# Performance work log

Measured on AMD Instinct MI355X. Metric: run time of the kernel, lower is better.

The kernel has to match this reference:

```python
import jax, jax.numpy as jnp
import numpy as np

DIM = 768
HEADS = 8
HEAD_DIM = DIM // HEADS  # 96, divisible by 6 for 3-axis RoPE
ROPE_BASE = 10000.0


def rotary_pe_3d(x, coords):
    """Apply 3D-coordinate rotary embedding.
    x: [B, h, L, d] with d % 6 == 0; coords: [B, L, 3].
    Head dim is split into 3 equal blocks, one per spatial axis; each block
    gets rotate-half RoPE with angle = coord_axis * inv_freq.
    """
    B, h, L, d = x.shape
    d3 = d // 3
    half = d3 // 2
    inv_freq = 1.0 / (ROPE_BASE ** (jnp.arange(half, dtype=x.dtype) / half))  # [half]
    ang = coords[..., None] * inv_freq  # [B, L, 3, half]
    cos = jnp.cos(ang)[:, None]  # [B, 1, L, 3, half]
    sin = jnp.sin(ang)[:, None]
    xr = x.reshape(B, h, L, 3, d3)
    x1, x2 = xr[..., :half], xr[..., half:]
    out = jnp.concatenate([x1 * cos - x2 * sin, x1 * sin + x2 * cos], axis=-1)
    return out.reshape(B, h, L, d)


def setup_inputs() -> dict:
    key = jax.random.key(0)
    ks = jax.random.split(key, 9)
    B, Lq, Lk = 2, 2048, 2048
    s = DIM ** -0.5
    return {
        "Q_in": jax.random.normal(ks[0], (B, Lq, DIM), jnp.float32),
        "K_in": jax.random.normal(ks[1], (B, Lk, DIM), jnp.float32),
        "V_in": jax.random.normal(ks[2], (B, Lk, DIM), jnp.float32),
        "coords_q": jax.random.uniform(ks[3], (B, Lq, 3), jnp.float32) * 10.0,
        "coords_k": jax.random.uniform(ks[4], (B, Lk, 3), jnp.float32) * 10.0,
        "Wq": jax.random.normal(ks[5], (DIM, DIM), jnp.float32) * s,
        "Wk": jax.random.normal(ks[6], (DIM, DIM), jnp.float32) * s,
        "Wv": jax.random.normal(ks[7], (DIM, DIM), jnp.float32) * s,
        "Wo": jax.random.normal(ks[8], (DIM, DIM), jnp.float32) * s,
    }


def _split_heads(x, h):
    B, L, C = x.shape
    return x.reshape(B, L, h, C // h).transpose(0, 2, 1, 3)  # [B,h,L,d]


def reference(Q_in, K_in, V_in, coords_q, coords_k, Wq, Wk, Wv, Wo):
    scale = HEAD_DIM ** -0.5
    q = _split_heads(Q_in @ Wq.T, HEADS)
    k = _split_heads(K_in @ Wk.T, HEADS)
    v = _split_heads(V_in @ Wv.T, HEADS)
    q = rotary_pe_3d(q, coords_q)
    k = rotary_pe_3d(k, coords_k)
    attn = jnp.einsum('bhqd,bhkd->bhqk', q, k) * scale
    attn = jax.nn.softmax(attn, axis=-1)
    out = jnp.einsum('bhqk,bhkd->bhqd', attn, v)
    B, h, L, d = out.shape
    out = out.transpose(0, 2, 1, 3).reshape(B, L, h * d)
    return out @ Wo.T
```

## Files before the change

### kernel.cpp

```cpp
#include <hip/hip_runtime.h>
#include <stdint.h>

#define H 8
#define DH 96
#define L 2048
#define NB 2
#define D 768
#define ACTE 3145728
#define WELE 589824

typedef unsigned short u16;
typedef unsigned int u32;
typedef __attribute__((ext_vector_type(4))) __bf16 bf16x4;
typedef __attribute__((ext_vector_type(8))) __bf16 bf16x8;
typedef __attribute__((ext_vector_type(4))) float f32x4;
typedef __attribute__((ext_vector_type(16))) float f32x16;
typedef __attribute__((ext_vector_type(4))) u32 u32x4;
typedef __attribute__((ext_vector_type(2))) u32 u32x2;
typedef __attribute__((ext_vector_type(4))) u16 u16x4;

#define QSCALE 0.14724444f

static __device__ __forceinline__ u16 f2bf(float f) {
  union { __bf16 h; u16 u; } v;
  v.h = (__bf16)f;
  return v.u;
}

static __device__ __forceinline__ bf16x8 cvt8r(f32x4 a, f32x4 b) {
  bf16x8 r;
  r[0] = (__bf16)a[0]; r[1] = (__bf16)a[1]; r[2] = (__bf16)a[2]; r[3] = (__bf16)a[3];
  r[4] = (__bf16)b[0]; r[5] = (__bf16)b[1]; r[6] = (__bf16)b[2]; r[7] = (__bf16)b[3];
  return r;
}

static __device__ __forceinline__ void bar_lds() {
  asm volatile("s_waitcnt lgkmcnt(0)" ::: "memory");
  __builtin_amdgcn_s_barrier();
}

__global__ __launch_bounds__(256)
void cvt_bf16(const float* __restrict__ q, const float* __restrict__ k,
              const float* __restrict__ v, const float* __restrict__ wq,
              const float* __restrict__ wk, const float* __restrict__ wv,
              u16* __restrict__ dst)
{
  const long NCH = (3L * ACTE + 3L * WELE) / 8;
  for (long c = (long)blockIdx.x * 256 + threadIdx.x; c < NCH;
       c += (long)gridDim.x * 256) {
    long e = c * 8;
    const float* s;
    if (e < 3L * ACTE) {
      int t = (int)(e / ACTE);
      s = (t == 0 ? q : (t == 1 ? k : v)) + (e - (long)t * ACTE);
    } else {
      long e2 = e - 3L * ACTE;
      int t = (int)(e2 / WELE);
      s = (t == 0 ? wq : (t == 1 ? wk : wv)) + (e2 - (long)t * WELE);
    }
    f32x4 a = *(const f32x4*)s;
    f32x4 b = *(const f32x4*)(s + 4);
    *(bf16x8*)(dst + e) = cvt8r(a, b);
  }
}

__global__ __launch_bounds__(256, 3)
void proj_qkv_b(const u16* __restrict__ bfb,
                const float* __restrict__ cq, const float* __restrict__ ck,
                u16* __restrict__ qo, u16* __restrict__ ko, u16* __restrict__ vo)
{
  __shared__ __attribute__((aligned(16))) u16 a_lds[128 * 32];
  __shared__ __attribute__((aligned(16))) u16 b_lds[128 * 32];
  const int tid = threadIdx.x;
  const int lane = tid & 63;
  const int w = tid >> 6;
  const int wr = w >> 1, wc = w & 1;
  const int fr = lane & 15;
  const int hi = lane >> 4;

  const int f = blockIdx.x;
  const int xr = f & 7;
  const int g = f >> 3;
  const int z = g / 24;
  const int gg = g % 24;
  const int by = xr + 8 * (gg & 3);
  const int bx = gg >> 2;
  const int row0 = by * 128;
  const int col0 = bx * 128;

  const u16* A = bfb + (size_t)z * ACTE;
  const u16* W = bfb + 3L * ACTE + (size_t)z * WELE;

  f32x4 acc[4][4] = {};

  const int lrow = lane >> 2;
  const int lcol = (lane & 3) * 8;
  auto dma = [&](int k0) {
#pragma unroll
    for (int j = 0; j < 2; j++) {
      const int r0 = w * 32 + j * 16;
      const u16* gpa = A + (size_t)(row0 + r0 + lrow) * D + k0 + lcol;
      const u16* gpb = W + (size_t)(col0 + r0 + lrow) * D + k0 + lcol;
      __builtin_amdgcn_global_load_lds(
          (const __attribute__((address_space(1))) u32*)gpa,
          (__attribute__((address_space(3))) u32*)&a_lds[r0 * 32], 16, 0, 0);
      __builtin_amdgcn_global_load_lds(
          (const __attribute__((address_space(1))) u32*)gpb,
          (__attribute__((address_space(3))) u32*)&b_lds[r0 * 32], 16, 0, 0);
    }
  };

#pragma unroll 1
  for (int k0 = 0; k0 < D; k0 += 32) {
    dma(k0);
    __syncthreads();
    bf16x8 af[4], bf[4];
#pragma unroll
    for (int m = 0; m < 4; m++)
      af[m] = *(const bf16x8*)(&a_lds[(wr * 64 + m * 16 + fr) * 32 + hi * 8]);
#pragma unroll
    for (int n = 0; n < 4; n++)
      bf[n] = *(const bf16x8*)(&b_lds[(wc * 64 + n * 16 + fr) * 32 + hi * 8]);
#pragma unroll
    for (int m = 0; m < 4; m++)
#pragma unroll
      for (int n = 0; n < 4; n++)
        acc[m][n] = __builtin_amdgcn_mfma_f32_16x16x32_bf16(af[m], bf[n], acc[m][n], 0, 0, 0);
    __syncthreads();
  }

  if (z == 2) {
#pragma unroll
    for (int m = 0; m < 4; m++) {
      int rbase = row0 + wr * 64 + m * 16 + hi * 4;
#pragma unroll
      for (int n = 0; n < 4; n++) {
        int c = col0 + wc * 64 + n * 16 + fr;
        int hh = c / DH, dd = c % DH;
#pragma unroll
        for (int r = 0; r < 4; r++) {
          int row = rbase + r;
          int b = row >> 11, l = row & (L - 1);
          vo[((size_t)((b * H + hh) * DH + dd)) * L + l] = f2bf(acc[m][n][r]);
        }
      }
    }
  } else {
    const float* coords = (z == 0) ? cq : ck;
    u16* outp = (z == 0) ? qo : ko;
    const float postscale = (z == 0) ? QSCALE : 1.0f;
#pragma unroll
    for (int m = 0; m < 4; m++) {
      int rbase = row0 + wr * 64 + m * 16 + hi * 4;
#pragma unroll
      for (int np = 0; np < 2; np++) {
        int n1 = np * 2;
        int c1 = col0 + wc * 64 + n1 * 16 + fr;
        int hh = c1 / DH;
        int dd1 = c1 % DH;
        int axis = dd1 / 32;
        int j = dd1 & 15;
        float invf = exp2f(-(float)j * 0.83048202372184058f);
#pragma unroll
        for (int r = 0; r < 4; r++) {
          int row = rbase + r;
          int b = row >> 11, l = row & (L - 1);
          float coord = coords[((size_t)(b * L + l)) * 3 + axis];
          float ang = coord * invf;
          float sn = __sinf(ang), cs = __cosf(ang);
          float x1 = acc[m][n1][r], x2 = acc[m][n1 + 1][r];
          size_t base = ((size_t)((b * H + hh) * L + l)) * DH;
          outp[base + dd1] = f2bf((x1 * cs - x2 * sn) * postscale);
          outp[base + dd1 + 16] = f2bf((x1 * sn + x2 * cs) * postscale);
        }
      }
    }
  }
}

__global__ __launch_bounds__(256, 3)
void proj_qkv(const float* __restrict__ Qin, const float* __restrict__ Kin,
              const float* __restrict__ Vin,
              const float* __restrict__ Wq, const float* __restrict__ Wk,
              const float* __restrict__ Wv,
              const float* __restrict__ cq, const float* __restrict__ ck,
              u16* __restrict__ qo, u16* __restrict__ ko, u16* __restrict__ vo)
{
  __shared__ u16 a_lds[2][64 * 40];
  __shared__ u16 b_lds[2][192 * 40];
  const int tid = threadIdx.x;
  const int lane = tid & 63;
  const int w = tid >> 6;
  const int wr = w >> 1, wc = w & 1;
  const int fr = lane & 15;
  const int hi = lane >> 4;

  const int f = blockIdx.x;
  const int xcd = f & 7;
  const int g = f >> 3;
  const int bx = g & 3;
  const int h2 = g >> 2;
  const int byp = h2 & 7;
  const int z = h2 >> 3;
  const int by = xcd + 8 * byp;
  const int row0 = by * 64;
  const int col0 = bx * 192;

  const float* A = (z == 0) ? Qin : ((z == 1) ? Kin : Vin);
  const float* W = (z == 0) ? Wq : ((z == 1) ? Wk : Wv);

  const int arow = tid >> 2;
  const int acol = (tid & 3) * 8;
  const float* pA = A + (size_t)(row0 + arow) * D + acol;
  const float* pB0 = W + (size_t)(col0 + arow) * D + acol;
  const float* pB1 = pB0 + (size_t)64 * D;
  const float* pB2 = pB0 + (size_t)128 * D;

  f32x4 acc[2][6] = {};
  f32x4 Sa[2], Sb[6], Ta[2], Tb[6];

  auto issueP = [&](int k, f32x4* ra, f32x4* rb) {
    ra[0] = *(const f32x4*)(pA + k);
    ra[1] = *(const f32x4*)(pA + k + 4);
    rb[0] = *(const f32x4*)(pB0 + k);
    rb[1] = *(const f32x4*)(pB0 + k + 4);
    rb[2] = *(const f32x4*)(pB1 + k);
    rb[3] = *(const f32x4*)(pB1 + k + 4);
    rb[4] = *(const f32x4*)(pB2 + k);
    rb[5] = *(const f32x4*)(pB2 + k + 4);
  };
  auto stageP = [&](int bi, const f32x4* ra, const f32x4* rb) {
    *(bf16x8*)(&a_lds[bi][arow * 40 + acol]) = cvt8r(ra[0], ra[1]);
    *(bf16x8*)(&b_lds[bi][arow * 40 + acol]) = cvt8r(rb[0], rb[1]);
    *(bf16x8*)(&b_lds[bi][(arow + 64) * 40 + acol]) = cvt8r(rb[2], rb[3]);
    *(bf16x8*)(&b_lds[bi][(arow + 128) * 40 + acol]) = cvt8r(rb[4], rb[5]);
  };
  auto compute = [&](int bi) {
    bf16x8 af[2], bf[6];
#pragma unroll
    for (int m = 0; m < 2; m++)
      af[m] = *(const bf16x8*)(&a_lds[bi][(wr * 32 + m * 16 + fr) * 40 + hi * 8]);
#pragma unroll
    for (int n = 0; n < 6; n++)
      bf[n] = *(const bf16x8*)(&b_lds[bi][(wc * 96 + n * 16 + fr) * 40 + hi * 8]);
#pragma unroll
    for (int m = 0; m < 2; m++)
#pragma unroll
      for (int n = 0; n < 6; n++)
        acc[m][n] = __builtin_amdgcn_mfma_f32_16x16x32_bf16(af[m], bf[n], acc[m][n], 0, 0, 0);
  };

  issueP(0, Sa, Sb);
  stageP(0, Sa, Sb);
  issueP(32, Ta, Tb);
  bar_lds();

#pragma unroll 1
  for (int tt = 0; tt < 12; tt++) {
    const int k2 = tt * 64;
    if (k2 + 64 < D) issueP(k2 + 64, Sa, Sb);
    compute(0);
    stageP(1, Ta, Tb);
    bar_lds();
    if (k2 + 96 < D) issueP(k2 + 96, Ta, Tb);
    compute(1);
    if (k2 + 64 < D) stageP(0, Sa, Sb);
    bar_lds();
  }

  const int hh = (col0 + wc * 96) / DH;
  if (z == 2) {
#pragma unroll
    for (int m = 0; m < 2; m++) {
      int rbase = row0 + wr * 32 + m * 16 + hi * 4;
#pragma unroll
      for (int n = 0; n < 6; n++) {
        int dd = n * 16 + fr;
#pragma unroll
        for (int r = 0; r < 4; r++) {
          int row = rbase + r;
          int b = row >> 11, l = row & (L - 1);
          vo[((size_t)((b * H + hh) * DH + dd)) * L + l] = f2bf(acc[m][n][r]);
        }
      }
    }
  } else {
    const float* coords = (z == 0) ? cq : ck;
    u16* outp = (z == 0) ? qo : ko;
    const float postscale = (z == 0) ? QSCALE : 1.0f;
    const float invf = exp2f(-(float)fr * 0.83048202372184058f);
#pragma unroll
    for (int m = 0; m < 2; m++) {
      int rbase = row0 + wr * 32 + m * 16 + hi * 4;
#pragma unroll
      for (int np = 0; np < 3; np++) {
        int n1 = np * 2;
        int dd1 = n1 * 16 + fr;
#pragma unroll
        for (int r = 0; r < 4; r++) {
          int row = rbase + r;
          int b = row >> 11, l = row & (L - 1);
          float coord = coords[((size_t)(b * L + l)) * 3 + np];
          float ang = coord * invf;
          float sn = __sinf(ang), cs = __cosf(ang);
          float x1 = acc[m][n1][r], x2 = acc[m][n1 + 1][r];
          size_t base = ((size_t)((b * H + hh) * L + l)) * DH;
          outp[base + dd1] = f2bf((x1 * cs - x2 * sn) * postscale);
          outp[base + dd1 + 16] = f2bf((x1 * sn + x2 * cs) * postscale);
        }
      }
    }
  }
}

#define KSTR 104
#define VSTR 72
#define NT   (L / 64)
__global__ __launch_bounds__(256, 3)
void attn_fwd(const u16* __restrict__ q_ws, const u16* __restrict__ k_ws,
              const u16* __restrict__ vt_ws, u16* __restrict__ ao)
{
  __shared__ __attribute__((aligned(16))) u16 k_lds[2][64 * KSTR];
  __shared__ __attribute__((aligned(16))) u16 vt_lds[2][96 * VSTR];
  const int tid = threadIdx.x;
  const int lane = tid & 63;
  const int w = tid >> 6;

  const int f = blockIdx.x;
  const int xr = f & 7;
  const int g = f >> 3;
  const int qx = g & 31;
  const int bh = xr + 8 * (g >> 5);
  const int q0 = qx * 64;

  const int qlo = lane & 31;
  const int hi32 = lane >> 5;
  const int wq = w >> 1;
  const int kk0 = (w & 1) * 32;

  const u16* kbase = k_ws + (size_t)bh * L * DH;
  const u16* vtbase = vt_ws + (size_t)bh * DH * L;

  const int perm[4] = {0, 2, 1, 3};

  int kg_off[3], kl0[3], kl1[3];
  int vg_off[3], vl0[3], vl1[3];
#pragma unroll
  for (int it = 0; it < 3; it++) {
    int ch = tid + it * 256;
    int krow = ch / 12, dc = ch % 12;
    kg_off[it] = krow * DH + dc * 8;
    int c0 = dc * 2;
    kl0[it] = krow * KSTR + (c0 >> 2) * 16 + perm[c0 & 3] * 4;
    kl1[it] = krow * KSTR + (c0 >> 2) * 16 + perm[(c0 + 1) & 3] * 4;
    int vrow = ch >> 3, vq = (ch & 7) * 2;
    vg_off[it] = vrow * L + vq * 4;
    vl0[it] = vrow * VSTR + (vq >> 2) * 16 + perm[vq & 3] * 4;
    vl1[it] = vrow * VSTR + (vq >> 2) * 16 + perm[(vq + 1) & 3] * 4;
  }

  bf16x8 qf[6];
  {
    const u16* qb = q_ws + ((size_t)bh * L + q0 + wq * 32 + qlo) * DH;
#pragma unroll
    for (int s = 0; s < 6; s++) {
      bf16x4 a = *(const bf16x4*)(qb + s * 16 + hi32 * 4);
      bf16x4 b = *(const bf16x4*)(qb + s * 16 + hi32 * 4 + 8);
      bf16x8 q;
      q[0] = a[0]; q[1] = a[1]; q[2] = a[2]; q[3] = a[3];
      q[4] = b[0]; q[5] = b[1]; q[6] = b[2]; q[7] = b[3];
      qf[s] = q;
    }
  }

  f32x16 o[3] = {};
  float m_r = -1e30f, l_r = 0.f;

  u32x4 kreg[3], vreg[3];
  auto kissue = [&](int t) {
    const u16* kb = kbase + (size_t)t * 64 * DH;
    const u16* vb = vtbase + t * 64;
#pragma unroll
    for (int it = 0; it < 3; it++) {
      kreg[it] = *(const u32x4*)(kb + kg_off[it]);
      vreg[it] = *(const u32x4*)(vb + vg_off[it]);
    }
  };
  auto kwrite = [&](int bi) {
#pragma unroll
    for (int it = 0; it < 3; it++) {
      u32x2 klo = { kreg[it][0], kreg[it][1] };
      u32x2 khi = { kreg[it][2], kreg[it][3] };
      *(u32x2*)(&k_lds[bi][kl0[it]]) = klo;
      *(u32x2*)(&k_lds[bi][kl1[it]]) = khi;
      u32x2 vlo = { vreg[it][0], vreg[it][1] };
      u32x2 vhi = { vreg[it][2], vreg[it][3] };
      *(u32x2*)(&vt_lds[bi][vl0[it]]) = vlo;
      *(u32x2*)(&vt_lds[bi][vl1[it]]) = vhi;
    }
  };

  kissue(0);
  kwrite(0);
  __syncthreads();

  int cur = 0;
  for (int t = 0; t < NT; t++) {
    if (t + 1 < NT) kissue(t + 1);

    f32x16 s2 = {};
#pragma unroll
    for (int s = 0; s < 6; s++) {
      bf16x8 kfrag = *(const bf16x8*)(
          &k_lds[cur][(kk0 + qlo) * KSTR + s * 16 + hi32 * 8]);
      s2 = __builtin_amdgcn_mfma_f32_32x32x16_bf16(kfrag, qf[s], s2, 0, 0, 0);
    }

    float a0 = fmaxf(fmaxf(s2[0], s2[1]), s2[2]);
    float a1 = fmaxf(fmaxf(s2[3], s2[4]), s2[5]);
    float a2 = fmaxf(fmaxf(s2[6], s2[7]), s2[8]);
    float a3 = fmaxf(fmaxf(s2[9], s2[10]), s2[11]);
    float a4 = fmaxf(fmaxf(s2[12], s2[13]), s2[14]);
    float pmax = fmaxf(fmaxf(fmaxf(a0, a1), a2), fmaxf(fmaxf(a3, a4), s2[15]));
    if (!__all(pmax - m_r <= 8.0f)) {
      float mx = fmaxf(pmax, __shfl_xor(pmax, 32));
      float mn = fmaxf(m_r, mx);
      float alpha = exp2f(m_r - mn);
      m_r = mn;
      l_r *= alpha;
#pragma unroll
      for (int db = 0; db < 3; db++)
#pragma unroll
        for (int r = 0; r < 16; r++)
          o[db][r] *= alpha;
    }

    float p[16];
    float rs = 0.f;
#pragma unroll
    for (int r = 0; r < 16; r++) {
      p[r] = exp2f(s2[r] - m_r);
      rs += p[r];
    }
    l_r += rs;

    bf16x8 pt[2];
#pragma unroll
    for (int s = 0; s < 2; s++)
#pragma unroll
      for (int j = 0; j < 8; j++)
        pt[s][j] = (__bf16)p[s * 8 + j];

#pragma unroll
    for (int s = 0; s < 2; s++)
#pragma unroll
      for (int db = 0; db < 3; db++) {
        bf16x8 vfrag = *(const bf16x8*)(
            &vt_lds[cur][(db * 32 + qlo) * VSTR + kk0 + s * 16 + hi32 * 8]);
        o[db] = __builtin_amdgcn_mfma_f32_32x32x16_bf16(vfrag, pt[s], o[db], 0, 0, 0);
      }

    if (t + 1 < NT) {
      kwrite(cur ^ 1);
      __syncthreads();
      cur ^= 1;
    }
  }

  float l_w = l_r + __shfl_xor(l_r, 32);

  {
    float* xb = (float*)&k_lds[wq][0];
    const int base = lane * 52;
    if (w & 1) {
#pragma unroll
      for (int db = 0; db < 3; db++)
#pragma unroll
        for (int rg = 0; rg < 4; rg++) {
          f32x4 v = { o[db][rg * 4], o[db][rg * 4 + 1],
                      o[db][rg * 4 + 2], o[db][rg * 4 + 3] };
          *(f32x4*)&xb[base + db * 16 + rg * 4] = v;
        }
      xb[base + 48] = m_r;
      xb[base + 49] = l_w;
    }
    __syncthreads();
    if (!(w & 1)) {
      float m1 = xb[base + 48], l1 = xb[base + 49];
      float ms = fmaxf(m_r, m1);
      float c0 = exp2f(m_r - ms), c1 = exp2f(m1 - ms);
      float inv = 1.f / (l_w * c0 + l1 * c1);
      const int b = bh >> 3, hh = bh & 7;
      const int lrow = q0 + wq * 32 + qlo;
      u16* aop = ao + ((size_t)(b * L + lrow)) * D + hh * DH;
#pragma unroll
      for (int db = 0; db < 3; db++)
#pragma unroll
        for (int rg = 0; rg < 4; rg++) {
          f32x4 op = *(const f32x4*)&xb[base + db * 16 + rg * 4];
          u16x4 pk;
#pragma unroll
          for (int r4 = 0; r4 < 4; r4++)
            pk[r4] = f2bf((o[db][rg * 4 + r4] * c0 + op[r4] * c1) * inv);
          *(u16x4*)(aop + db * 32 + rg * 8 + hi32 * 4) = pk;
        }
    }
  }
}

__global__ __launch_bounds__(256, 3)
void gemm_out(const u16* __restrict__ A, const float* __restrict__ W,
              float* __restrict__ out)
{
  __shared__ u16 a_lds[2][64 * 40];
  __shared__ u16 b_lds[2][64 * 40];
  const int tid = threadIdx.x;
  const int lane = tid & 63;
  const int w = tid >> 6;
  const int wr = w >> 1, wc = w & 1;

  const int f = blockIdx.x;
  const int xr = f & 7;
  const int g = f >> 3;
  const int bx = g % 12;
  const int wq = g / 12;
  const int by = xr + 8 * wq;
  const int row0 = by * 64;
  const int col0 = bx * 64;

  f32x4 acc[2][2] = {};
  const int srow = tid >> 2;
  const int scol = (tid & 3) * 8;
  const u16* pA = A + (size_t)(row0 + srow) * D + scol;
  const float* pW = W + (size_t)(col0 + srow) * D + scol;
  const int fr = lane & 15;
  const int fk = (lane >> 4) * 8;

  auto issueG = [&](int k, u32x4* ra, f32x4* rb) {
    ra[0] = *(const u32x4*)(pA + k);
    rb[0] = *(const f32x4*)(pW + k);
    rb[1] = *(const f32x4*)(pW + k + 4);
  };
  auto writeG = [&](int bi, const u32x4* ra, const f32x4* rb) {
    *(u32x4*)(&a_lds[bi][srow * 40 + scol]) = ra[0];
    *(bf16x8*)(&b_lds[bi][srow * 40 + scol]) = cvt8r(rb[0], rb[1]);
  };
  auto computeG = [&](int bi) {
    bf16x8 af[2], bfr[2];
#pragma unroll
    for (int m = 0; m < 2; m++)
      af[m] = *(const bf16x8*)(&a_lds[bi][(wr * 32 + m * 16 + fr) * 40 + fk]);
#pragma unroll
    for (int n = 0; n < 2; n++)
      bfr[n] = *(const bf16x8*)(&b_lds[bi][(wc * 32 + n * 16 + fr) * 40 + fk]);
#pragma unroll
    for (int m = 0; m < 2; m++)
#pragma unroll
      for (int n = 0; n < 2; n++)
        acc[m][n] = __builtin_amdgcn_mfma_f32_16x16x32_bf16(af[m], bfr[n], acc[m][n], 0, 0, 0);
  };

  u32x4 raA[1], raB[1];
  f32x4 rbA[2], rbB[2];
  issueG(0, raB, rbB);
  writeG(0, raB, rbB);
  issueG(32, raA, rbA);
  __syncthreads();

  for (int k0 = 0; k0 < D; k0 += 64) {
    if (k0 + 64 < D) issueG(k0 + 64, raB, rbB);
    computeG(0);
    writeG(1, raA, rbA);
    __syncthreads();
    if (k0 + 96 < D) issueG(k0 + 96, raA, rbA);
    computeG(1);
    if (k0 + 64 < D) writeG(0, raB, rbB);
    __syncthreads();
  }

#pragma unroll
  for (int m = 0; m < 2; m++) {
    int rbase = row0 + wr * 32 + m * 16 + (lane >> 4) * 4;
#pragma unroll
    for (int n = 0; n < 2; n++) {
      int c = col0 + wc * 32 + n * 16 + fr;
#pragma unroll
      for (int r = 0; r < 4; r++)
        out[(size_t)(rbase + r) * D + c] = acc[m][n][r];
    }
  }
}

extern "C" void kernel_launch(void* const* d_in, const int* in_sizes, int n_in,
                              void* d_out, int out_size, void* d_ws, size_t ws_size,
                              hipStream_t stream) {
  (void)in_sizes; (void)n_in; (void)out_size;
  const float* Qin = (const float*)d_in[0];
  const float* Kin = (const float*)d_in[1];
  const float* Vin = (const float*)d_in[2];
  const float* cq  = (const float*)d_in[3];
  const float* ck  = (const float*)d_in[4];
  const float* Wq  = (const float*)d_in[5];
  const float* Wk  = (const float*)d_in[6];
  const float* Wv  = (const float*)d_in[7];
  const float* Wo  = (const float*)d_in[8];
  float* out = (float*)d_out;

  const size_t per = (size_t)NB * H * L * DH;
  const size_t base_need = 4 * per * sizeof(u16);
  const size_t scr_elems = 3L * ACTE + 3L * WELE;
  const size_t full_need = base_need + scr_elems * sizeof(u16);
  if (ws_size < base_need) return;

  u16* q_ws  = (u16*)d_ws;
  u16* k_ws  = q_ws + per;
  u16* vt_ws = k_ws + per;
  u16* ao_ws = vt_ws + per;

  if (ws_size >= full_need) {
    u16* bfb = ao_ws + per;
    cvt_bf16<<<dim3(2048), dim3(256), 0, stream>>>(Qin, Kin, Vin, Wq, Wk, Wv, bfb);
    proj_qkv_b<<<dim3(576), dim3(256), 0, stream>>>(bfb, cq, ck, q_ws, k_ws, vt_ws);
  } else {
    proj_qkv<<<dim3(768), dim3(256), 0, stream>>>(
        Qin, Kin, Vin, Wq, Wk, Wv, cq, ck, q_ws, k_ws, vt_ws);
  }
  attn_fwd<<<dim3(32 * NB * H), dim3(256), 0, stream>>>(q_ws, k_ws, vt_ws, ao_ws);
  gemm_out<<<dim3(12 * 64), dim3(256), 0, stream>>>(ao_ws, Wo, out);
}
```

Baseline: 99.34 us.

## Double-buffer LDS tiles in QKV projection GEMM to overlap loads with MFMA

```diff
diff --git a/kernel.cpp b/kernel.cpp
--- a/kernel.cpp
+++ b/kernel.cpp
@@ -69,8 +69,8 @@
                 const float* __restrict__ cq, const float* __restrict__ ck,
                 u16* __restrict__ qo, u16* __restrict__ ko, u16* __restrict__ vo)
 {
-  __shared__ __attribute__((aligned(16))) u16 a_lds[128 * 32];
-  __shared__ __attribute__((aligned(16))) u16 b_lds[128 * 32];
+  __shared__ __attribute__((aligned(16))) u16 a_lds[2][128 * 32];
+  __shared__ __attribute__((aligned(16))) u16 b_lds[2][128 * 32];
   const int tid = threadIdx.x;
   const int lane = tid & 63;
   const int w = tid >> 6;
@@ -95,7 +95,7 @@
 
   const int lrow = lane >> 2;
   const int lcol = (lane & 3) * 8;
-  auto dma = [&](int k0) {
+  auto dma = [&](int k0, int bi) {
 #pragma unroll
     for (int j = 0; j < 2; j++) {
       const int r0 = w * 32 + j * 16;
@@ -103,30 +103,42 @@
       const u16* gpb = W + (size_t)(col0 + r0 + lrow) * D + k0 + lcol;
       __builtin_amdgcn_global_load_lds(
           (const __attribute__((address_space(1))) u32*)gpa,
-          (__attribute__((address_space(3))) u32*)&a_lds[r0 * 32], 16, 0, 0);
+          (__attribute__((address_space(3))) u32*)&a_lds[bi][r0 * 32], 16, 0, 0);
       __builtin_amdgcn_global_load_lds(
           (const __attribute__((address_space(1))) u32*)gpb,
-          (__attribute__((address_space(3))) u32*)&b_lds[r0 * 32], 16, 0, 0);
-    }
-  };
-
+          (__attribute__((address_space(3))) u32*)&b_lds[bi][r0 * 32], 16, 0, 0);
+    }
+  };
+  auto compute = [&](int bi) {
+    bf16x8 af[4], bf[4];
+#pragma unroll
+    for (int m = 0; m < 4; m++)
+      af[m] = *(const bf16x8*)(&a_lds[bi][(wr * 64 + m * 16 + fr) * 32 + hi * 8]);
+#pragma unroll
+    for (int n = 0; n < 4; n++)
+      bf[n] = *(const bf16x8*)(&b_lds[bi][(wc * 64 + n * 16 + fr) * 32 + hi * 8]);
+#pragma unroll
+    for (int m = 0; m < 4; m++)
+#pragma unroll
+      for (int n = 0; n < 4; n++)
+        acc[m][n] = __builtin_amdgcn_mfma_f32_16x16x32_bf16(af[m], bf[n], acc[m][n], 0, 0, 0);
+  };
+
+  dma(0, 0);
+  int cur = 0;
 #pragma unroll 1
   for (int k0 = 0; k0 < D; k0 += 32) {
-    dma(k0);
-    __syncthreads();
-    bf16x8 af[4], bf[4];
-#pragma unroll
-    for (int m = 0; m < 4; m++)
-      af[m] = *(const bf16x8*)(&a_lds[(wr * 64 + m * 16 + fr) * 32 + hi * 8]);
-#pragma unroll
-    for (int n = 0; n < 4; n++)
-      bf[n] = *(const bf16x8*)(&b_lds[(wc * 64 + n * 16 + fr) * 32 + hi * 8]);
-#pragma unroll
-    for (int m = 0; m < 4; m++)
-#pragma unroll
-      for (int n = 0; n < 4; n++)
-        acc[m][n] = __builtin_amdgcn_mfma_f32_16x16x32_bf16(af[m], bf[n], acc[m][n], 0, 0, 0);
-    __syncthreads();
+    if (k0 + 32 < D) {
+      dma(k0 + 32, cur ^ 1);
+      asm volatile("s_waitcnt vmcnt(4)" ::: "memory");
+    } else {
+      asm volatile("s_waitcnt vmcnt(0)" ::: "memory");
+    }
+    __builtin_amdgcn_sched_barrier(0);
+    __builtin_amdgcn_s_barrier();
+    compute(cur);
+    bar_lds();
+    cur ^= 1;
   }
 
   if (z == 2) {
```

After: 99.40 us. No clear change (+0.1%).
